# Kernel optimization log

Measured on AMD Instinct MI355X. Metric: run time of the kernel, lower is better.

Reference implementation:

```python
import jax, jax.numpy as jnp
import numpy as np
from jax import lax

THRESHOLD = 1.25
CURRENT_DECAY = 0.25   # lava-dl convention: cur = (1 - decay)*cur + z
VOLTAGE_DECAY = 0.25
TAU_GRAD = 0.1
SCALE_GRAD = 1.0
WEIGHT_SCALE = 2.0

@jax.custom_vjp
def spike(v):
    return (v >= THRESHOLD).astype(v.dtype)

def _spike_fwd(v):
    return spike(v), v

def _spike_bwd(v, g):
    # slayer exponential surrogate gradient around the threshold
    return (g * SCALE_GRAD * jnp.exp(-jnp.abs(v - THRESHOLD) / TAU_GRAD),)

spike.defvjp(_spike_fwd, _spike_bwd)

def lif_scan(z):
    # z: [T, B, N] synaptic input; CUBA LIF with zero-reset on spike
    B, N = z.shape[1], z.shape[2]
    init = (jnp.zeros((B, N), z.dtype), jnp.zeros((B, N), z.dtype))
    def step(carry, zt):
        cur, vol = carry
        cur = (1.0 - CURRENT_DECAY) * cur + zt
        vol = (1.0 - VOLTAGE_DECAY) * vol + cur
        s = spike(vol)
        vol = vol * (1.0 - s)  # reset to 0 on spike
        return (cur, vol), s
    _, spikes = lax.scan(step, init, z)
    return spikes  # [T, B, N]

def apply_delay(s, d):
    # s: [T, B, N]; d: [N] int per-neuron axonal delay. out[t] = s[t - d] (zero-padded)
    T = s.shape[0]
    t_idx = jnp.arange(T)[:, None] - d[None, :]          # [T, N]
    valid = (t_idx >= 0).astype(s.dtype)                  # [T, N]
    idx = jnp.broadcast_to(jnp.clip(t_idx, 0, T - 1)[:, None, :], s.shape)
    return jnp.take_along_axis(s, idx, axis=0) * valid[:, None, :]

def dense_block(s, w, d=None):
    # s: [T, B, in]; w: [out, in]
    z = jnp.einsum('tbi,oi->tbo', s, w) * WEIGHT_SCALE
    s = lif_scan(z)
    if d is not None:
        s = apply_delay(s, d)
    return s

def setup_inputs() -> dict:
    key = jax.random.key(0)
    k = jax.random.split(key, 6)
    B, T = 128, 1024
    x = (jax.random.uniform(k[0], (B, 64, T)) < 0.2).astype(jnp.float32)  # binary input spikes
    w1 = jax.random.normal(k[1], (256, 64), jnp.float32) * 0.1
    w2 = jax.random.normal(k[2], (256, 256), jnp.float32) * 0.1
    w3 = jax.random.normal(k[3], (11, 256), jnp.float32) * 0.1
    d1 = jax.random.randint(k[4], (256,), 0, 8, jnp.int32)
    d2 = jax.random.randint(k[5], (256,), 0, 8, jnp.int32)
    return {"x": x, "w1": w1, "w2": w2, "w3": w3, "d1": d1, "d2": d2}

def reference(x, w1, w2, w3, d1, d2):
    s = jnp.transpose(x, (2, 0, 1))  # [B,C,T] -> [T,B,C]
    s = dense_block(s, w1, d1)
    s = dense_block(s, w2, d2)
    s = dense_block(s, w3, None)
    return jnp.transpose(s, (1, 2, 0))  # [B, num_classes, T]
```

## Files before the change

### kernel.cpp

```cpp
#include <hip/hip_runtime.h>

#define T_STEPS 1024
#define BATCH 128

using u16 = unsigned short;

__device__ __forceinline__ float bf2f(u16 u) {
  union { unsigned int i; float f; } c; c.i = ((unsigned int)u) << 16; return c.f;
}

__global__ __launch_bounds__(256) void k_transpose(const float* __restrict__ x,
                                                   u16* __restrict__ s0) {
  __shared__ float tile[64][65];
  const int b = blockIdx.y, t0 = blockIdx.x * 64, tid = threadIdx.x;
  {
    const int tt = tid & 63, ic = tid >> 6;
#pragma unroll
    for (int ii = 0; ii < 16; ++ii) {
      const int i = ic * 16 + ii;
      tile[i][tt] = x[((size_t)b * 64 + i) * T_STEPS + t0 + tt];
    }
  }
  __syncthreads();
  {
    const int i = tid & 63, tc = tid >> 6;
#pragma unroll
    for (int jj = 0; jj < 16; ++jj) {
      const int t = tc * 16 + jj;
      const float v = tile[i][t];
      s0[((size_t)b * T_STEPS + t0 + t) * 64 + i] = (u16)(__float_as_uint(v) >> 16);
    }
  }
}

template <int K>
__global__ __launch_bounds__(256) void k_gemm(const u16* __restrict__ S,
                                              const float* __restrict__ W,
                                              float* __restrict__ Z) {
  __shared__ float sA[32][132];
  __shared__ float sB[32][132];
  const int m0 = blockIdx.x * 128, o0 = blockIdx.y * 128;
  const int tid = threadIdx.x;
  const int tx = tid & 15, ty = tid >> 4;
  const int sr = tid >> 1;
  const int kh = (tid & 1) * 16;
  float acc[8][8] = {};
  for (int kk = 0; kk < K; kk += 32) {
    const uint4 av0 = *(const uint4*)(S + (size_t)(m0 + sr) * K + kk + kh);
    const uint4 av1 = *(const uint4*)(S + (size_t)(m0 + sr) * K + kk + kh + 8);
    const float4 bv0 = *(const float4*)(W + (size_t)(o0 + sr) * K + kk + kh);
    const float4 bv1 = *(const float4*)(W + (size_t)(o0 + sr) * K + kk + kh + 4);
    const float4 bv2 = *(const float4*)(W + (size_t)(o0 + sr) * K + kk + kh + 8);
    const float4 bv3 = *(const float4*)(W + (size_t)(o0 + sr) * K + kk + kh + 12);
    __syncthreads();
    {
      const u16* ap = (const u16*)&av0;
#pragma unroll
      for (int j = 0; j < 8; ++j) sA[kh + j][sr] = bf2f(ap[j]);
      const u16* aq = (const u16*)&av1;
#pragma unroll
      for (int j = 0; j < 8; ++j) sA[kh + 8 + j][sr] = bf2f(aq[j]);
      const float* bp = (const float*)&bv0;
#pragma unroll
      for (int j = 0; j < 4; ++j) sB[kh + j][sr] = bp[j];
      const float* bq = (const float*)&bv1;
#pragma unroll
      for (int j = 0; j < 4; ++j) sB[kh + 4 + j][sr] = bq[j];
      const float* br = (const float*)&bv2;
#pragma unroll
      for (int j = 0; j < 4; ++j) sB[kh + 8 + j][sr] = br[j];
      const float* bs = (const float*)&bv3;
#pragma unroll
      for (int j = 0; j < 4; ++j) sB[kh + 12 + j][sr] = bs[j];
    }
    __syncthreads();
#pragma unroll
    for (int k = 0; k < 32; ++k) {
      float a[8], b[8];
      *(float4*)&a[0] = *(const float4*)&sA[k][ty * 4];
      *(float4*)&a[4] = *(const float4*)&sA[k][64 + ty * 4];
      *(float4*)&b[0] = *(const float4*)&sB[k][tx * 4];
      *(float4*)&b[4] = *(const float4*)&sB[k][64 + tx * 4];
#pragma unroll
      for (int i = 0; i < 8; ++i)
#pragma unroll
        for (int j = 0; j < 8; ++j) acc[i][j] += a[i] * b[j];
    }
  }
#pragma unroll
  for (int i = 0; i < 8; ++i) {
    const int row = m0 + (i < 4 ? ty * 4 + i : 64 + ty * 4 + (i - 4));
    float4 lo, hi;
    lo.x = 2.f * acc[i][0];
    lo.y = 2.f * acc[i][1];
    lo.z = 2.f * acc[i][2];
    lo.w = 2.f * acc[i][3];
    hi.x = 2.f * acc[i][4];
    hi.y = 2.f * acc[i][5];
    hi.z = 2.f * acc[i][6];
    hi.w = 2.f * acc[i][7];
    float* zr = Z + (size_t)row * 256 + o0;
    *(float4*)(zr + tx * 4) = lo;
    *(float4*)(zr + 64 + tx * 4) = hi;
  }
}

__global__ __launch_bounds__(256) void k_gemm_out(const u16* __restrict__ S,
                                                  const float* __restrict__ W3,
                                                  float* __restrict__ Z3) {
  __shared__ u16 sS[64 * 264];
  const int m0 = blockIdx.x * 64;
  const int tid = threadIdx.x;
#pragma unroll
  for (int c = 0; c < 8; ++c) {
    const int e = (c * 256 + tid) * 8;
    const int r = e >> 8, k = e & 255;
    *reinterpret_cast<uint4*>(&sS[r * 264 + k]) =
        *reinterpret_cast<const uint4*>(S + (size_t)(m0 + r) * 256 + k);
  }
  __syncthreads();
  const int ml = tid & 63, og = tid >> 6;
  const u16* row = &sS[ml * 264];
  const float* w0 = W3 + og * 256;
  const float* w1 = W3 + (og + 4) * 256;
  const float* w2p = W3 + (size_t)(og + 8 < 11 ? og + 8 : og) * 256;
  float acc0 = 0.f, acc1 = 0.f, acc2 = 0.f;
  for (int k = 0; k < 256; ++k) {
    const float sv = bf2f(row[k]);
    acc0 += sv * w0[k];
    acc1 += sv * w1[k];
    acc2 += sv * w2p[k];
  }
  float* zr = Z3 + (size_t)(m0 + ml) * 16;
  zr[og] = 2.f * acc0;
  zr[og + 4] = 2.f * acc1;
  if (og + 8 < 11) zr[og + 8] = 2.f * acc2;
}

template <int CH, int STR>
__device__ __forceinline__ void load_chunk(const float* __restrict__ zp, int base,
                                           float (&zb)[CH]) {
#pragma unroll
  for (int u = 0; u < CH; ++u) zb[u] = zp[(size_t)(base + u) * STR];
}

__global__ __launch_bounds__(128) void k_scan_delay(const float* __restrict__ Z,
                                                    u16* __restrict__ Sout,
                                                    const int* __restrict__ d) {
  const int b = blockIdx.x >> 1, nh = blockIdx.x & 1;
  const int n = (nh << 7) + threadIdx.x;
  const int del = d[n];
  const float* zp = Z + (size_t)b * T_STEPS * 256 + n;
  u16* sp = Sout + (size_t)b * T_STEPS * 256 + n;
  for (int t = 0; t < del; ++t) sp[(size_t)t * 256] = 0;
  const int tmax = T_STEPS - del;
  float cur = 0.f, vol = 0.f;
  float zA[32], zB[32];
  load_chunk<32, 256>(zp, 0, zA);
  for (int c = 0; c < 32; c += 2) {
    if (c + 1 < 32) load_chunk<32, 256>(zp, (c + 1) * 32, zB);
#pragma unroll
    for (int u = 0; u < 32; ++u) {
      const int t = c * 32 + u;
      cur = 0.75f * cur + zA[u];
      vol = 0.75f * vol + cur;
      const bool s = vol >= 1.25f;
      vol = s ? 0.f : vol;
      if (t < tmax) sp[(size_t)(t + del) * 256] = s ? (u16)0x3F80 : (u16)0;
    }
    if (c + 2 < 32) load_chunk<32, 256>(zp, (c + 2) * 32, zA);
#pragma unroll
    for (int u = 0; u < 32; ++u) {
      const int t = (c + 1) * 32 + u;
      cur = 0.75f * cur + zB[u];
      vol = 0.75f * vol + cur;
      const bool s = vol >= 1.25f;
      vol = s ? 0.f : vol;
      if (t < tmax) sp[(size_t)(t + del) * 256] = s ? (u16)0x3F80 : (u16)0;
    }
  }
}

__global__ __launch_bounds__(64) void k_scan_out(const float* __restrict__ Z3,
                                                 float* __restrict__ out) {
  const int b = blockIdx.x, o = threadIdx.x;
  if (o >= 11) return;
  const float* zp = Z3 + (size_t)b * T_STEPS * 16 + o;
  float* op = out + ((size_t)b * 11 + o) * T_STEPS;
  float cur = 0.f, vol = 0.f;
  float zA[32], zB[32], ob[4];
  load_chunk<32, 16>(zp, 0, zA);
  for (int c = 0; c < 32; c += 2) {
    if (c + 1 < 32) load_chunk<32, 16>(zp, (c + 1) * 32, zB);
#pragma unroll
    for (int u = 0; u < 32; ++u) {
      cur = 0.75f * cur + zA[u];
      vol = 0.75f * vol + cur;
      const bool s = vol >= 1.25f;
      vol = s ? 0.f : vol;
      ob[u & 3] = s ? 1.f : 0.f;
      if ((u & 3) == 3)
        *reinterpret_cast<float4*>(op + c * 32 + (u - 3)) =
            make_float4(ob[0], ob[1], ob[2], ob[3]);
    }
    if (c + 2 < 32) load_chunk<32, 16>(zp, (c + 2) * 32, zA);
#pragma unroll
    for (int u = 0; u < 32; ++u) {
      cur = 0.75f * cur + zB[u];
      vol = 0.75f * vol + cur;
      const bool s = vol >= 1.25f;
      vol = s ? 0.f : vol;
      ob[u & 3] = s ? 1.f : 0.f;
      if ((u & 3) == 3)
        *reinterpret_cast<float4*>(op + (c + 1) * 32 + (u - 3)) =
            make_float4(ob[0], ob[1], ob[2], ob[3]);
    }
  }
}

extern "C" void kernel_launch(void* const* d_in, const int* in_sizes, int n_in,
                              void* d_out, int out_size, void* d_ws, size_t ws_size,
                              hipStream_t stream) {
  const float* x = (const float*)d_in[0];
  const float* w1 = (const float*)d_in[1];
  const float* w2 = (const float*)d_in[2];
  const float* w3 = (const float*)d_in[3];
  const int* d1 = (const int*)d_in[4];
  const int* d2 = (const int*)d_in[5];
  float* out = (float*)d_out;

  const int M = BATCH * T_STEPS;
  float* Z = (float*)d_ws;
  u16* Sb = (u16*)((char*)d_ws + (size_t)M * 256 * 4);

  k_transpose<<<dim3(T_STEPS / 64, BATCH), 256, 0, stream>>>(x, Sb);
  k_gemm<64><<<dim3(M / 128, 2), 256, 0, stream>>>(Sb, w1, Z);
  k_scan_delay<<<BATCH * 2, 128, 0, stream>>>(Z, Sb, d1);
  k_gemm<256><<<dim3(M / 128, 2), 256, 0, stream>>>(Sb, w2, Z);
  k_scan_delay<<<BATCH * 2, 128, 0, stream>>>(Z, Sb, d2);
  k_gemm_out<<<M / 64, 256, 0, stream>>>(Sb, w3, Z);
  k_scan_out<<<BATCH, 64, 0, stream>>>(Z, out);
}
```

Measured before the change: 416.7 us.

## Fuse input transpose into first GEMM and widen GEMM tile to full output width

Removes the separate transpose kernel: the first GEMM reads x directly in [B,C,T] layout and writes it into shared memory already in k-major order. Both GEMMs now compute all 256 outputs per block (128x256 tile, 8x16 accumulators per thread), so the A operand is loaded only once rather than once for each output half. In exchange, register pressure rises sharply (128 accumulators per thread) and shared memory grows, which may limit occupancy despite the launch_bounds hint; the grid is also halved.

```diff
diff --git a/kernel.cpp b/kernel.cpp
--- a/kernel.cpp
+++ b/kernel.cpp
@@ -9,99 +9,85 @@
   union { unsigned int i; float f; } c; c.i = ((unsigned int)u) << 16; return c.f;
 }
 
-__global__ __launch_bounds__(256) void k_transpose(const float* __restrict__ x,
-                                                   u16* __restrict__ s0) {
-  __shared__ float tile[64][65];
-  const int b = blockIdx.y, t0 = blockIdx.x * 64, tid = threadIdx.x;
-  {
-    const int tt = tid & 63, ic = tid >> 6;
-#pragma unroll
-    for (int ii = 0; ii < 16; ++ii) {
-      const int i = ic * 16 + ii;
-      tile[i][tt] = x[((size_t)b * 64 + i) * T_STEPS + t0 + tt];
-    }
-  }
-  __syncthreads();
-  {
-    const int i = tid & 63, tc = tid >> 6;
-#pragma unroll
-    for (int jj = 0; jj < 16; ++jj) {
-      const int t = tc * 16 + jj;
-      const float v = tile[i][t];
-      s0[((size_t)b * T_STEPS + t0 + t) * 64 + i] = (u16)(__float_as_uint(v) >> 16);
-    }
-  }
-}
-
-template <int K>
-__global__ __launch_bounds__(256) void k_gemm(const u16* __restrict__ S,
-                                              const float* __restrict__ W,
-                                              float* __restrict__ Z) {
-  __shared__ float sA[32][132];
-  __shared__ float sB[32][132];
-  const int m0 = blockIdx.x * 128, o0 = blockIdx.y * 128;
+template <int K, bool XSRC>
+__global__ __launch_bounds__(256, 2) void k_gemm(const u16* __restrict__ S,
+                                                 const float* __restrict__ W,
+                                                 float* __restrict__ Z,
+                                                 const float* __restrict__ x) {
+  __shared__ float sA[32][136];
+  __shared__ float sB[32][264];
+  const int m0 = blockIdx.x * 128;
   const int tid = threadIdx.x;
   const int tx = tid & 15, ty = tid >> 4;
-  const int sr = tid >> 1;
-  const int kh = (tid & 1) * 16;
-  float acc[8][8] = {};
+
+  float acc[8][16] = {};
+#pragma unroll 1
   for (int kk = 0; kk < K; kk += 32) {
-    const uint4 av0 = *(const uint4*)(S + (size_t)(m0 + sr) * K + kk + kh);
-    const uint4 av1 = *(const uint4*)(S + (size_t)(m0 + sr) * K + kk + kh + 8);
-    const float4 bv0 = *(const float4*)(W + (size_t)(o0 + sr) * K + kk + kh);
-    const float4 bv1 = *(const float4*)(W + (size_t)(o0 + sr) * K + kk + kh + 4);
-    const float4 bv2 = *(const float4*)(W + (size_t)(o0 + sr) * K + kk + kh + 8);
-    const float4 bv3 = *(const float4*)(W + (size_t)(o0 + sr) * K + kk + kh + 12);
+    float4 bw[8];
+    {
+      const float* wp = W + (size_t)tid * K + kk;
+#pragma unroll
+      for (int c = 0; c < 8; ++c) bw[c] = *(const float4*)(wp + c * 4);
+    }
+    if constexpr (XSRC) {
+      const int b = m0 >> 10, t0 = m0 & 1023;
+      const int kq = tid >> 3, seg = tid & 7;
+      const float* xp = x + ((size_t)b * 64 + kk + kq) * T_STEPS + t0 + seg * 16;
+      float4 v0 = *(const float4*)(xp + 0);
+      float4 v1 = *(const float4*)(xp + 4);
+      float4 v2 = *(const float4*)(xp + 8);
+      float4 v3 = *(const float4*)(xp + 12);
+      __syncthreads();
+      *(float4*)&sA[kq][seg * 16 + 0] = v0;
+      *(float4*)&sA[kq][seg * 16 + 4] = v1;
+      *(float4*)&sA[kq][seg * 16 + 8] = v2;
+      *(float4*)&sA[kq][seg * 16 + 12] = v3;
+    } else {
+      const int sr = tid >> 1, kh = (tid & 1) * 16;
+      const uint4 a0 = *(const uint4*)(S + (size_t)(m0 + sr) * K + kk + kh);
+      const uint4 a1 = *(const uint4*)(S + (size_t)(m0 + sr) * K + kk + kh + 8);
+      __syncthreads();
+      const u16* ap = (const u16*)&a0;
+#pragma unroll
+      for (int j = 0; j < 8; ++j) sA[kh + j][sr] = bf2f(ap[j]);
+      const u16* aq = (const u16*)&a1;
+#pragma unroll
+      for (int j = 0; j < 8; ++j) sA[kh + 8 + j][sr] = bf2f(aq[j]);
+    }
+    {
+      const float* bp = (const float*)&bw[0];
+#pragma unroll
+      for (int j = 0; j < 32; ++j) sB[j][tid] = bp[j];
+    }
     __syncthreads();
-    {
-      const u16* ap = (const u16*)&av0;
-#pragma unroll
-      for (int j = 0; j < 8; ++j) sA[kh + j][sr] = bf2f(ap[j]);
-      const u16* aq = (const u16*)&av1;
-#pragma unroll
-      for (int j = 0; j < 8; ++j) sA[kh + 8 + j][sr] = bf2f(aq[j]);
-      const float* bp = (const float*)&bv0;
-#pragma unroll
-      for (int j = 0; j < 4; ++j) sB[kh + j][sr] = bp[j];
-      const float* bq = (const float*)&bv1;
-#pragma unroll
-      for (int j = 0; j < 4; ++j) sB[kh + 4 + j][sr] = bq[j];
-      const float* br = (const float*)&bv2;
-#pragma unroll
-      for (int j = 0; j < 4; ++j) sB[kh + 8 + j][sr] = br[j];
-      const float* bs = (const float*)&bv3;
-#pragma unroll
-      for (int j = 0; j < 4; ++j) sB[kh + 12 + j][sr] = bs[j];
-    }
-    __syncthreads();
-#pragma unroll
+#pragma unroll 2
     for (int k = 0; k < 32; ++k) {
-      float a[8], b[8];
+      float a[8], b[16];
       *(float4*)&a[0] = *(const float4*)&sA[k][ty * 4];
       *(float4*)&a[4] = *(const float4*)&sA[k][64 + ty * 4];
       *(float4*)&b[0] = *(const float4*)&sB[k][tx * 4];
       *(float4*)&b[4] = *(const float4*)&sB[k][64 + tx * 4];
+      *(float4*)&b[8] = *(const float4*)&sB[k][128 + tx * 4];
+      *(float4*)&b[12] = *(const float4*)&sB[k][192 + tx * 4];
 #pragma unroll
       for (int i = 0; i < 8; ++i)
 #pragma unroll
-        for (int j = 0; j < 8; ++j) acc[i][j] += a[i] * b[j];
+        for (int j = 0; j < 16; ++j) acc[i][j] += a[i] * b[j];
     }
   }
 #pragma unroll
   for (int i = 0; i < 8; ++i) {
     const int row = m0 + (i < 4 ? ty * 4 + i : 64 + ty * 4 + (i - 4));
-    float4 lo, hi;
-    lo.x = 2.f * acc[i][0];
-    lo.y = 2.f * acc[i][1];
-    lo.z = 2.f * acc[i][2];
-    lo.w = 2.f * acc[i][3];
-    hi.x = 2.f * acc[i][4];
-    hi.y = 2.f * acc[i][5];
-    hi.z = 2.f * acc[i][6];
-    hi.w = 2.f * acc[i][7];
-    float* zr = Z + (size_t)row * 256 + o0;
-    *(float4*)(zr + tx * 4) = lo;
-    *(float4*)(zr + 64 + tx * 4) = hi;
+    float* zr = Z + (size_t)row * 256;
+#pragma unroll
+    for (int c = 0; c < 4; ++c) {
+      float4 v;
+      v.x = 2.f * acc[i][c * 4 + 0];
+      v.y = 2.f * acc[i][c * 4 + 1];
+      v.z = 2.f * acc[i][c * 4 + 2];
+      v.w = 2.f * acc[i][c * 4 + 3];
+      *(float4*)(zr + c * 64 + tx * 4) = v;
+    }
   }
 }
 
@@ -233,10 +219,9 @@
   float* Z = (float*)d_ws;
   u16* Sb = (u16*)((char*)d_ws + (size_t)M * 256 * 4);
 
-  k_transpose<<<dim3(T_STEPS / 64, BATCH), 256, 0, stream>>>(x, Sb);
-  k_gemm<64><<<dim3(M / 128, 2), 256, 0, stream>>>(Sb, w1, Z);
+  k_gemm<64, true><<<M / 128, 256, 0, stream>>>(Sb, w1, Z, x);
   k_scan_delay<<<BATCH * 2, 128, 0, stream>>>(Z, Sb, d1);
-  k_gemm<256><<<dim3(M / 128, 2), 256, 0, stream>>>(Sb, w2, Z);
+  k_gemm<256, false><<<M / 128, 256, 0, stream>>>(Sb, w2, Z, x);
   k_scan_delay<<<BATCH * 2, 128, 0, stream>>>(Z, Sb, d2);
   k_gemm_out<<<M / 64, 256, 0, stream>>>(Sb, w3, Z);
   k_scan_out<<<BATCH, 64, 0, stream>>>(Z, out);
```

After: 426.1 us. 2.2% more time.
